# Optimization experiments

Measured on AMD Instinct MI355X. Metric: run time of the kernel, lower is better.

## Reference

```python
import jax, jax.numpy as jnp
import numpy as np

VOCAB, X_SIZE, H_SIZE, N_CLASSES = 50000, 300, 150, 5
DEPTH = 18                      # complete binary tree, N = 2^(DEPTH+1)-1 nodes
N_NODES = 2 ** (DEPTH + 1) - 1  # 524287
SCALE = 0.05                    # param init scale for numerical sanity


def setup_inputs() -> dict:
    key = jax.random.key(0)
    ks = jax.random.split(key, 8)
    return {
        "x_id": jax.random.randint(ks[0], (N_NODES,), 0, VOCAB, dtype=jnp.int32),
        "emb": jax.random.normal(ks[1], (VOCAB, X_SIZE), jnp.float32) * SCALE,
        "W_iou": jax.random.normal(ks[2], (X_SIZE, 3 * H_SIZE), jnp.float32) * SCALE,
        "U_iou": jax.random.normal(ks[3], (H_SIZE, 3 * H_SIZE), jnp.float32) * SCALE,
        "b_iou": jnp.zeros((3 * H_SIZE,), jnp.float32),
        "W_f": jax.random.normal(ks[4], (X_SIZE, H_SIZE), jnp.float32) * SCALE,
        "U_f": jax.random.normal(ks[5], (H_SIZE, H_SIZE), jnp.float32) * SCALE,
        "b_f": jnp.zeros((H_SIZE,), jnp.float32),
        "W_out": jax.random.normal(ks[6], (H_SIZE, N_CLASSES), jnp.float32) * SCALE,
        "b_out": jnp.zeros((N_CLASSES,), jnp.float32),
    }


def reference(x_id, emb, W_iou, U_iou, b_iou, W_f, U_f, b_f, W_out, b_out):
    # Child-Sum TreeLSTM propagated leaves->root over a complete binary tree
    # stored in heap layout: children of node i are 2i+1, 2i+2.
    N = x_id.shape[0]
    H = U_iou.shape[0]
    depth = int(np.log2(N + 1)) - 1

    x = emb[x_id]  # input_module: embedding lookup  [N, X]
    h = jnp.zeros((N, H), x.dtype)
    c = jnp.zeros((N, H), x.dtype)

    # level-batched topological propagation (19 static levels)
    for lvl in range(depth, -1, -1):
        s, e = 2 ** lvl - 1, 2 ** (lvl + 1) - 1  # node range of this level
        xl = x[s:e]                              # [n_l, X]
        if lvl == depth:  # leaves: zero child state
            h_sum = jnp.zeros((e - s, H), x.dtype)
            fc_sum = jnp.zeros((e - s, H), x.dtype)
        else:
            # children of consecutive nodes are contiguous: [2s+1, 2e+1)
            hc = h[2 * s + 1:2 * e + 1].reshape(e - s, 2, H)
            cc = c[2 * s + 1:2 * e + 1].reshape(e - s, 2, H)
            h_sum = hc.sum(axis=1)               # reduce: sum child h
            # per-child forget gate
            f = jax.nn.sigmoid((xl @ W_f)[:, None, :] + hc @ U_f + b_f)
            fc_sum = (f * cc).sum(axis=1)
        iou = xl @ W_iou + h_sum @ U_iou + b_iou  # [n_l, 3H]
        i, o, u = jnp.split(iou, 3, axis=-1)
        c_new = jax.nn.sigmoid(i) * jnp.tanh(u) + fc_sum
        h_new = jax.nn.sigmoid(o) * jnp.tanh(c_new)
        h = h.at[s:e].set(h_new)
        c = c.at[s:e].set(c_new)

    return h @ W_out + b_out  # output_module: Linear(H, C)  [N, C]
```

## Files before the change

### kernel.cpp

```cpp
#include <hip/hip_runtime.h>
#include <cstdint>

typedef _Float16 f16_t;
typedef __attribute__((ext_vector_type(8))) _Float16 f16x8;
typedef __attribute__((ext_vector_type(4))) _Float16 f16x4;
typedef __attribute__((ext_vector_type(4))) float f32x4;

#define HP      160
#define NCOL    640
#define KXP     320
#define LEAF_S  262143
#define NVOCAB  50000
#define AST     168
#define BST     36
#define CST     162

__device__ __forceinline__ float frcp(float x) { return __builtin_amdgcn_rcpf(x); }
__device__ __forceinline__ float sigf(float x) { return frcp(1.0f + __expf(-x)); }
__device__ __forceinline__ float tanhf_(float x) {
  return 1.0f - 2.0f * frcp(1.0f + __expf(2.0f * x));
}
__device__ __forceinline__ f16x8 zero8() {
  f16x8 z;
#pragma unroll
  for (int i = 0; i < 8; ++i) z[i] = (_Float16)0.0f;
  return z;
}
__device__ __forceinline__ f32x4 zero4() {
  f32x4 z;
#pragma unroll
  for (int i = 0; i < 4; ++i) z[i] = 0.0f;
  return z;
}

__device__ __forceinline__ void stage_B(const f16_t* __restrict__ UreT, f16_t* B_sh,
                                        int tid, int j0, int kk) {
#pragma unroll
  for (int i = 0; i < 2; ++i) {
    int ch = tid + 256 * i;
    int cidx = ch >> 2, kc = (ch & 3) * 8;
    int g = cidx >> 5, jj = cidx & 31;
    int col = g * HP + j0 + jj;
    f16x8 v = *(const f16x8*)&UreT[col * HP + kk + kc];
    f16x4 lo = {v[0], v[1], v[2], v[3]};
    f16x4 hi = {v[4], v[5], v[6], v[7]};
    *(f16x4*)&B_sh[cidx * BST + kc] = lo;
    *(f16x4*)&B_sh[cidx * BST + kc + 4] = hi;
  }
}
__device__ __forceinline__ f16x8 read_B(const f16_t* B_sh, int tile16, int q) {
  f16x4 lo = *(const f16x4*)&B_sh[tile16 * BST + q * 8];
  f16x4 hi = *(const f16x4*)&B_sh[tile16 * BST + q * 8 + 4];
  f16x8 v = {lo[0], lo[1], lo[2], lo[3], hi[0], hi[1], hi[2], hi[3]};
  return v;
}

__global__ void prep_params(const float* __restrict__ W_iou, const float* __restrict__ U_iou,
                            const float* __restrict__ b_iou, const float* __restrict__ W_f,
                            const float* __restrict__ U_f, const float* __restrict__ b_f,
                            f16_t* __restrict__ WreT, f16_t* __restrict__ UreT,
                            float* __restrict__ bre) {
  int idx = blockIdx.x * 256 + threadIdx.x;
  if (idx < NCOL * KXP) {
    int col = idx / KXP, k = idx % KXP;
    int j = col >> 2, g = col & 3;
    float v = 0.0f;
    if (k < 300 && j < 150) v = (g < 3) ? W_iou[k * 450 + g * 150 + j] : W_f[k * 150 + j];
    WreT[idx] = (f16_t)v;
  } else if (idx < NCOL * KXP + NCOL * HP) {
    int i2 = idx - NCOL * KXP;
    int col = i2 / HP, k = i2 % HP;
    int g = col / 160, j = col % 160;
    float v = 0.0f;
    if (k < 150 && j < 150) v = (g < 3) ? U_iou[k * 450 + g * 150 + j] : U_f[k * 150 + j];
    UreT[i2] = (f16_t)v;
  } else if (idx < NCOL * KXP + NCOL * HP + NCOL) {
    int col = idx - (NCOL * KXP + NCOL * HP);
    int j = col >> 2, g = col & 3;
    bre[col] = (j < 150) ? ((g < 3) ? b_iou[g * 150 + j] : b_f[j]) : 0.0f;
  }
}

__global__ __launch_bounds__(256) void gemm_p(const float* __restrict__ emb,
                                              const f16_t* __restrict__ WreT,
                                              const float* __restrict__ bre,
                                              f16_t* __restrict__ P) {
  __shared__ __align__(16) f16_t A_sh[64 * 328];
  __shared__ __align__(16) f16_t B_sh[128 * 40];
  const int tid = threadIdx.x;
  const int wid = tid >> 6, lane = tid & 63, l15 = lane & 15, q = lane >> 4;
  const int row0 = blockIdx.x * 64;

#pragma unroll
  for (int i = 0; i < 10; ++i) {
    int ch = tid + 256 * i;
    int r = ch / 40, kc = (ch % 40) * 8;
    int grow = row0 + r;
    f16x8 hv;
    if (grow < NVOCAB && kc + 8 <= 300) {
      float4 a = *(const float4*)&emb[grow * 300 + kc];
      float4 b = *(const float4*)&emb[grow * 300 + kc + 4];
      hv[0] = (_Float16)a.x; hv[1] = (_Float16)a.y; hv[2] = (_Float16)a.z; hv[3] = (_Float16)a.w;
      hv[4] = (_Float16)b.x; hv[5] = (_Float16)b.y; hv[6] = (_Float16)b.z; hv[7] = (_Float16)b.w;
    } else {
#pragma unroll
      for (int e = 0; e < 8; ++e) {
        int k = kc + e;
        float v = (grow < NVOCAB && k < 300) ? emb[grow * 300 + k] : 0.0f;
        hv[e] = (_Float16)v;
      }
    }
    *(f16x8*)&A_sh[r * 328 + kc] = hv;
  }
  __syncthreads();

  for (int bn = 0; bn < 5; ++bn) {
    const int col0 = bn * 128;
    f32x4 acc[8];
#pragma unroll
    for (int t = 0; t < 8; ++t) acc[t] = zero4();
    for (int kk = 0; kk < KXP; kk += 32) {
#pragma unroll
      for (int i = 0; i < 2; ++i) {
        int ch = tid + 256 * i;
        int cidx = ch >> 2, kc = (ch & 3) * 8;
        *(f16x8*)&B_sh[cidx * 40 + kc] =
            *(const f16x8*)&WreT[(col0 + cidx) * KXP + kk + kc];
      }
      __syncthreads();
      f16x8 af = *(const f16x8*)&A_sh[(16 * wid + l15) * 328 + kk + q * 8];
#pragma unroll
      for (int t = 0; t < 8; ++t) {
        f16x8 bfr = *(const f16x8*)&B_sh[(t * 16 + l15) * 40 + q * 8];
        acc[t] = __builtin_amdgcn_mfma_f32_16x16x32_f16(af, bfr, acc[t], 0, 0, 0);
      }
      __syncthreads();
    }
#pragma unroll
    for (int t = 0; t < 8; ++t) {
      int col = col0 + t * 16 + l15;
      float bias = bre[col];
#pragma unroll
      for (int r2 = 0; r2 < 4; ++r2) {
        int row = row0 + 16 * wid + q * 4 + r2;
        if (row < NVOCAB) P[(long)row * NCOL + col] = (f16_t)(acc[t][r2] + bias);
      }
    }
  }
}

__global__ void leafhc_kernel(const f16_t* __restrict__ P, f16_t* __restrict__ Hleaf,
                              f16_t* __restrict__ Cleaf) {
  int idx = blockIdx.x * 256 + threadIdx.x;
  if (idx >= NVOCAB * 80) return;
  int v = idx / 80, t = idx % 80;
  f16x8 pk = *(const f16x8*)&P[(long)v * NCOL + t * 8];
#pragma unroll
  for (int e = 0; e < 2; ++e) {
    float iv = (float)pk[e * 4 + 0], ov = (float)pk[e * 4 + 1], uv = (float)pk[e * 4 + 2];
    float cl = sigf(iv) * tanhf_(uv);
    float hl = sigf(ov) * tanhf_(cl);
    Hleaf[(long)v * HP + t * 2 + e] = (f16_t)hl;
    Cleaf[(long)v * HP + t * 2 + e] = (f16_t)cl;
  }
}

__global__ __launch_bounds__(256, 4) void fused17_kernel(
    const int* __restrict__ x_id, const f16_t* __restrict__ P,
    const f16_t* __restrict__ UreT, const f16_t* __restrict__ Hleaf,
    const f16_t* __restrict__ Cleaf, f16_t* __restrict__ Hout,
    f16_t* __restrict__ Cout, const float* __restrict__ W_out,
    const float* __restrict__ b_out, float* __restrict__ out) {
  __shared__ __align__(16) f16_t B_sh[128 * BST];
  __shared__ __align__(16) f16_t A2_sh[32 * AST];
  __shared__ f16_t C_sh[32 * CST];
  __shared__ __align__(16) f16_t Wo16[160 * 8];
  const int tid = threadIdx.x;
  const int wid = tid >> 6, lane = tid & 63, l15 = lane & 15, q = lane >> 4;
  const int p0 = blockIdx.x * 32;
  const int s1 = (1 << 17) - 1;
  const long childbase = (long)LEAF_S + 2 * p0;

  for (int idx = tid; idx < 1280; idx += 256) {
    int j = idx >> 3, m = idx & 7;
    Wo16[idx] = (j < 150 && m < 5) ? (f16_t)W_out[j * 5 + m] : (f16_t)0.0f;
  }

  const int row = 16 * wid + l15;
  const int xvrow = x_id[childbase + row];
  const f16_t* hrow = Hleaf + (long)xvrow * HP;
  f16x8 areg[5];
#pragma unroll
  for (int kx = 0; kx < 5; ++kx) areg[kx] = *(const f16x8*)&hrow[kx * 32 + q * 8];

  int xvp[2], xvl[2], xvr[2];
#pragma unroll
  for (int rr = 0; rr < 2; ++rr) {
    int pl = 8 * wid + 2 * q + rr;
    xvp[rr] = x_id[(long)s1 + p0 + pl];
    xvl[rr] = x_id[childbase + 2 * pl];
    xvr[rr] = x_id[childbase + 2 * pl + 1];
  }
  __syncthreads();

  {
    float o[5] = {0, 0, 0, 0, 0};
#pragma unroll
    for (int kx = 0; kx < 5; ++kx)
#pragma unroll
      for (int e = 0; e < 8; ++e) {
        int j = kx * 32 + q * 8 + e;
        float hv = (float)areg[kx][e];
        f16x8 w8 = *(const f16x8*)&Wo16[j * 8];
#pragma unroll
        for (int m = 0; m < 5; ++m) o[m] += hv * (float)w8[m];
      }
#pragma unroll
    for (int m = 0; m < 5; ++m) {
      float v = o[m];
      v += __shfl_xor(v, 16);
      v += __shfl_xor(v, 32);
      o[m] = v;
    }
    if (q == 0) {
      long base = (childbase + row) * 5;
#pragma unroll
      for (int m = 0; m < 5; ++m) out[base + m] = o[m] + b_out[m];
    }
  }

  float oacc1[2][5] = {};
  for (int jt = 0; jt < 5; ++jt) {
    const int j0 = jt * 32;
    f32x4 acc[4][2];
#pragma unroll
    for (int g = 0; g < 4; ++g)
#pragma unroll
      for (int jh = 0; jh < 2; ++jh) acc[g][jh] = zero4();

    for (int kx = 0; kx < 5; ++kx) {
      stage_B(UreT, B_sh, tid, j0, kx * 32);
      __syncthreads();
#pragma unroll
      for (int g = 0; g < 4; ++g)
#pragma unroll
        for (int jh = 0; jh < 2; ++jh) {
          f16x8 bfr = read_B(B_sh, g * 32 + jh * 16 + l15, q);
          acc[g][jh] = __builtin_amdgcn_mfma_f32_16x16x32_f16(areg[kx], bfr, acc[g][jh], 0, 0, 0);
        }
      __syncthreads();
    }

#pragma unroll
    for (int rr = 0; rr < 2; ++rr) {
      const int r = rr * 2;
      const int pl = 8 * wid + 2 * q + rr;
      const f16_t* Prp = P + (long)xvp[rr] * NCOL;
      const f16_t* Crl = Cleaf + (long)xvl[rr] * HP;
      const f16_t* Crr = Cleaf + (long)xvr[rr] * HP;
#pragma unroll
      for (int jh = 0; jh < 2; ++jh) {
        const int j = j0 + jh * 16 + l15;
        f16x4 pp = *(const f16x4*)&Prp[j * 4];
        float ipre = (float)pp[0] + acc[0][jh][r] + acc[0][jh][r + 1];
        float opre = (float)pp[1] + acc[1][jh][r] + acc[1][jh][r + 1];
        float upre = (float)pp[2] + acc[2][jh][r] + acc[2][jh][r + 1];
        float pf   = (float)pp[3];
        float fl = sigf(pf + acc[3][jh][r]);
        float fr = sigf(pf + acc[3][jh][r + 1]);
        float cn = sigf(ipre) * tanhf_(upre) + fl * (float)Crl[j] + fr * (float)Crr[j];
        float hn = sigf(opre) * tanhf_(cn);
        A2_sh[pl * AST + j] = (f16_t)hn;
        C_sh[pl * CST + j] = (f16_t)cn;
        f16x8 w8 = *(const f16x8*)&Wo16[j * 8];
#pragma unroll
        for (int m = 0; m < 5; ++m) oacc1[rr][m] += hn * (float)w8[m];
      }
    }
  }
  __syncthreads();

#pragma unroll
  for (int rr = 0; rr < 2; ++rr) {
    const int pl = 8 * wid + 2 * q + rr;
#pragma unroll
    for (int m = 0; m < 5; ++m) {
      float v = oacc1[rr][m];
      v += __shfl_xor(v, 1);
      v += __shfl_xor(v, 2);
      v += __shfl_xor(v, 4);
      v += __shfl_xor(v, 8);
      if (l15 == 0) out[((long)s1 + p0 + pl) * 5 + m] = v + b_out[m];
    }
  }

  const int s2 = (s1 - 1) >> 1;
  const int p02 = p0 >> 1;
  const bool act2 = (wid < 2);
  f16x8 a2reg[5];
  if (act2) {
#pragma unroll
    for (int kx = 0; kx < 5; ++kx)
      a2reg[kx] = *(const f16x8*)&A2_sh[(16 * wid + l15) * AST + kx * 32 + q * 8];
  }
  int xvp2[2];
#pragma unroll
  for (int rr = 0; rr < 2; ++rr) {
    int pl = 8 * wid + 2 * q + rr;
    xvp2[rr] = x_id[(long)s2 + p02 + (act2 ? pl : 0)];
  }

  float oacc2[2][5] = {};
  for (int jt = 0; jt < 5; ++jt) {
    const int j0 = jt * 32;
    f32x4 acc[4][2];
#pragma unroll
    for (int g = 0; g < 4; ++g)
#pragma unroll
      for (int jh = 0; jh < 2; ++jh) acc[g][jh] = zero4();

    for (int kx = 0; kx < 5; ++kx) {
      stage_B(UreT, B_sh, tid, j0, kx * 32);
      __syncthreads();
      if (act2) {
#pragma unroll
        for (int g = 0; g < 4; ++g)
#pragma unroll
          for (int jh = 0; jh < 2; ++jh) {
            f16x8 bfr = read_B(B_sh, g * 32 + jh * 16 + l15, q);
            acc[g][jh] = __builtin_amdgcn_mfma_f32_16x16x32_f16(a2reg[kx], bfr, acc[g][jh], 0, 0, 0);
          }
      }
      __syncthreads();
    }

    if (act2) {
#pragma unroll
      for (int rr = 0; rr < 2; ++rr) {
        const int r = rr * 2;
        const int lr0 = 16 * wid + q * 4 + r;
        const int pl = lr0 >> 1;
        const f16_t* Prp = P + (long)xvp2[rr] * NCOL;
#pragma unroll
        for (int jh = 0; jh < 2; ++jh) {
          const int j = j0 + jh * 16 + l15;
          f16x4 pp = *(const f16x4*)&Prp[j * 4];
          float ipre = (float)pp[0] + acc[0][jh][r] + acc[0][jh][r + 1];
          float opre = (float)pp[1] + acc[1][jh][r] + acc[1][jh][r + 1];
          float upre = (float)pp[2] + acc[2][jh][r] + acc[2][jh][r + 1];
          float pf   = (float)pp[3];
          float fl = sigf(pf + acc[3][jh][r]);
          float fr = sigf(pf + acc[3][jh][r + 1]);
          float cn = sigf(ipre) * tanhf_(upre) +
                     fl * (float)C_sh[lr0 * CST + j] + fr * (float)C_sh[(lr0 + 1) * CST + j];
          float hn = sigf(opre) * tanhf_(cn);
          Hout[(long)(p02 + pl) * HP + j] = (f16_t)hn;
          Cout[(long)(p02 + pl) * HP + j] = (f16_t)cn;
          f16x8 w8 = *(const f16x8*)&Wo16[j * 8];
#pragma unroll
          for (int m = 0; m < 5; ++m) oacc2[rr][m] += hn * (float)w8[m];
        }
      }
    }
  }

  if (act2) {
#pragma unroll
    for (int rr = 0; rr < 2; ++rr) {
      const int pl = 8 * wid + 2 * q + rr;
#pragma unroll
      for (int m = 0; m < 5; ++m) {
        float v = oacc2[rr][m];
        v += __shfl_xor(v, 1);
        v += __shfl_xor(v, 2);
        v += __shfl_xor(v, 4);
        v += __shfl_xor(v, 8);
        if (l15 == 0) out[((long)s2 + p02 + pl) * 5 + m] = v + b_out[m];
      }
    }
  }
}

__global__ __launch_bounds__(256, 4) void level_k(
    const int* __restrict__ x_id, const f16_t* __restrict__ P,
    const f16_t* __restrict__ UreT, const f16_t* __restrict__ Hc,
    const f16_t* __restrict__ Cc, f16_t* __restrict__ Hp,
    f16_t* __restrict__ Cp, const float* __restrict__ W_out,
    const float* __restrict__ b_out, float* __restrict__ out, int s, int M) {
  __shared__ __align__(16) f16_t B_sh[128 * BST];
  __shared__ __align__(16) f16_t Wo16[160 * 8];
  const int tid = threadIdx.x;
  const int wid = tid >> 6, lane = tid & 63, l15 = lane & 15, q = lane >> 4;
  const int p0 = blockIdx.x * 32;

  for (int idx = tid; idx < 1280; idx += 256) {
    int j = idx >> 3, m = idx & 7;
    Wo16[idx] = (j < 150 && m < 5) ? (f16_t)W_out[j * 5 + m] : (f16_t)0.0f;
  }

  const int row = 16 * wid + l15;
  const f16_t* hrow = Hc + (long)(2 * p0 + row) * HP;
  f16x8 areg[5];
#pragma unroll
  for (int kx = 0; kx < 5; ++kx) areg[kx] = *(const f16x8*)&hrow[kx * 32 + q * 8];

  int xvp[2];
#pragma unroll
  for (int rr = 0; rr < 2; ++rr) {
    int pl = 8 * wid + 2 * q + rr;
    xvp[rr] = x_id[(long)s + p0 + pl];
  }
  __syncthreads();

  float oacc[2][5] = {};
  for (int jt = 0; jt < 5; ++jt) {
    const int j0 = jt * 32;
    f32x4 acc[4][2];
#pragma unroll
    for (int g = 0; g < 4; ++g)
#pragma unroll
      for (int jh = 0; jh < 2; ++jh) acc[g][jh] = zero4();

    for (int kx = 0; kx < 5; ++kx) {
      stage_B(UreT, B_sh, tid, j0, kx * 32);
      __syncthreads();
#pragma unroll
      for (int g = 0; g < 4; ++g)
#pragma unroll
        for (int jh = 0; jh < 2; ++jh) {
          f16x8 bfr = read_B(B_sh, g * 32 + jh * 16 + l15, q);
          acc[g][jh] = __builtin_amdgcn_mfma_f32_16x16x32_f16(areg[kx], bfr, acc[g][jh], 0, 0, 0);
        }
      __syncthreads();
    }

#pragma unroll
    for (int rr = 0; rr < 2; ++rr) {
      const int r = rr * 2;
      const int lr0 = 16 * wid + q * 4 + r;
      const int pl = lr0 >> 1;
      const f16_t* Prp = P + (long)xvp[rr] * NCOL;
#pragma unroll
      for (int jh = 0; jh < 2; ++jh) {
        const int j = j0 + jh * 16 + l15;
        f16x4 pp = *(const f16x4*)&Prp[j * 4];
        float ipre = (float)pp[0] + acc[0][jh][r] + acc[0][jh][r + 1];
        float opre = (float)pp[1] + acc[1][jh][r] + acc[1][jh][r + 1];
        float upre = (float)pp[2] + acc[2][jh][r] + acc[2][jh][r + 1];
        float pf   = (float)pp[3];
        float fl = sigf(pf + acc[3][jh][r]);
        float fr = sigf(pf + acc[3][jh][r + 1]);
        float clv = (float)Cc[(long)(2 * p0 + lr0) * HP + j];
        float crv = (float)Cc[(long)(2 * p0 + lr0 + 1) * HP + j];
        float cn = sigf(ipre) * tanhf_(upre) + fl * clv + fr * crv;
        float hn = sigf(opre) * tanhf_(cn);
        Hp[(long)(p0 + pl) * HP + j] = (f16_t)hn;
        Cp[(long)(p0 + pl) * HP + j] = (f16_t)cn;
        f16x8 w8 = *(const f16x8*)&Wo16[j * 8];
#pragma unroll
        for (int m = 0; m < 5; ++m) oacc[rr][m] += hn * (float)w8[m];
      }
    }
  }

#pragma unroll
  for (int rr = 0; rr < 2; ++rr) {
    const int pl = 8 * wid + 2 * q + rr;
#pragma unroll
    for (int m = 0; m < 5; ++m) {
      float v = oacc[rr][m];
      v += __shfl_xor(v, 1);
      v += __shfl_xor(v, 2);
      v += __shfl_xor(v, 4);
      v += __shfl_xor(v, 8);
      if (l15 == 0) out[((long)s + p0 + pl) * 5 + m] = v + b_out[m];
    }
  }
}

__global__ __launch_bounds__(256, 4) void tail_kernel(
    const int* __restrict__ x_id, const f16_t* __restrict__ P,
    const f16_t* __restrict__ UreT, f16_t* __restrict__ HX, f16_t* __restrict__ HY,
    f16_t* __restrict__ CX, f16_t* __restrict__ CY, const float* __restrict__ W_out,
    const float* __restrict__ b_out, float* __restrict__ out) {
  __shared__ __align__(16) f16_t B_sh[128 * BST];
  __shared__ __align__(16) f16_t Wo16[160 * 8];
  const int tid = threadIdx.x;
  const int wid = tid >> 6, lane = tid & 63, l15 = lane & 15, q = lane >> 4;

  for (int idx = tid; idx < 1280; idx += 256) {
    int j = idx >> 3, m = idx & 7;
    Wo16[idx] = (j < 150 && m < 5) ? (f16_t)W_out[j * 5 + m] : (f16_t)0.0f;
  }

  for (int lvl = 5; lvl >= 0; --lvl) {
    const int s = (1 << lvl) - 1, M = 1 << lvl;
    const f16_t* hc = (lvl & 1) ? HX : HY;
    const f16_t* cc = (lvl & 1) ? CX : CY;
    f16_t* hp = (lvl & 1) ? HY : HX;
    f16_t* cp = (lvl & 1) ? CY : CX;
    int rowsValid = 2 * M;
    if (rowsValid > 64) rowsValid = 64;

    __threadfence();
    __syncthreads();

    const int row = 16 * wid + l15;
    f16x8 areg[5];
#pragma unroll
    for (int kx = 0; kx < 5; ++kx)
      areg[kx] = (row < rowsValid) ? *(const f16x8*)&hc[(long)row * HP + kx * 32 + q * 8]
                                   : zero8();

    int xvp[2]; bool valid[2];
#pragma unroll
    for (int rr = 0; rr < 2; ++rr) {
      int pl = 8 * wid + 2 * q + rr;
      valid[rr] = pl < M;
      xvp[rr] = x_id[(long)s + (valid[rr] ? pl : 0)];
    }

    float oacc[2][5] = {};
    for (int jt = 0; jt < 5; ++jt) {
      const int j0 = jt * 32;
      f32x4 acc[4][2];
#pragma unroll
      for (int g = 0; g < 4; ++g)
#pragma unroll
        for (int jh = 0; jh < 2; ++jh) acc[g][jh] = zero4();

      for (int kx = 0; kx < 5; ++kx) {
        stage_B(UreT, B_sh, tid, j0, kx * 32);
        __syncthreads();
#pragma unroll
        for (int g = 0; g < 4; ++g)
#pragma unroll
          for (int jh = 0; jh < 2; ++jh) {
            f16x8 bfr = read_B(B_sh, g * 32 + jh * 16 + l15, q);
            acc[g][jh] = __builtin_amdgcn_mfma_f32_16x16x32_f16(areg[kx], bfr, acc[g][jh], 0, 0, 0);
          }
        __syncthreads();
      }

#pragma unroll
      for (int rr = 0; rr < 2; ++rr) {
        const int r = rr * 2;
        const int lr0 = 16 * wid + q * 4 + r;
        const int pl = lr0 >> 1;
        const f16_t* Prp = P + (long)xvp[rr] * NCOL;
#pragma unroll
        for (int jh = 0; jh < 2; ++jh) {
          const int j = j0 + jh * 16 + l15;
          f16x4 pp = *(const f16x4*)&Prp[j * 4];
          float ipre = (float)pp[0] + acc[0][jh][r] + acc[0][jh][r + 1];
          float opre = (float)pp[1] + acc[1][jh][r] + acc[1][jh][r + 1];
          float upre = (float)pp[2] + acc[2][jh][r] + acc[2][jh][r + 1];
          float pf   = (float)pp[3];
          float fl = sigf(pf + acc[3][jh][r]);
          float fr = sigf(pf + acc[3][jh][r + 1]);
          float clv = valid[rr] ? (float)cc[(long)lr0 * HP + j] : 0.0f;
          float crv = valid[rr] ? (float)cc[(long)(lr0 + 1) * HP + j] : 0.0f;
          float cn = sigf(ipre) * tanhf_(upre) + fl * clv + fr * crv;
          float hn = sigf(opre) * tanhf_(cn);
          if (valid[rr]) {
            hp[(long)pl * HP + j] = (f16_t)hn;
            cp[(long)pl * HP + j] = (f16_t)cn;
          }
          f16x8 w8 = *(const f16x8*)&Wo16[j * 8];
#pragma unroll
          for (int m = 0; m < 5; ++m) oacc[rr][m] += hn * (float)w8[m];
        }
      }
    }

#pragma unroll
    for (int rr = 0; rr < 2; ++rr) {
      const int pl = 8 * wid + 2 * q + rr;
#pragma unroll
      for (int m = 0; m < 5; ++m) {
        float v = oacc[rr][m];
        v += __shfl_xor(v, 1);
        v += __shfl_xor(v, 2);
        v += __shfl_xor(v, 4);
        v += __shfl_xor(v, 8);
        if (l15 == 0 && valid[rr]) out[((long)s + pl) * 5 + m] = v + b_out[m];
      }
    }
  }
}

extern "C" void kernel_launch(void* const* d_in, const int* in_sizes, int n_in,
                              void* d_out, int out_size, void* d_ws, size_t ws_size,
                              hipStream_t stream) {
  const int* x_id   = (const int*)d_in[0];
  const float* emb  = (const float*)d_in[1];
  const float* W_iou = (const float*)d_in[2];
  const float* U_iou = (const float*)d_in[3];
  const float* b_iou = (const float*)d_in[4];
  const float* W_f   = (const float*)d_in[5];
  const float* U_f   = (const float*)d_in[6];
  const float* b_f   = (const float*)d_in[7];
  const float* W_out = (const float*)d_in[8];
  const float* b_out = (const float*)d_in[9];
  float* out = (float*)d_out;
  char* ws = (char*)d_ws;

  f16_t* WreT  = (f16_t*)(ws + 0);
  f16_t* UreT  = (f16_t*)(ws + 409600);
  float* bre   = (float*)(ws + 614400);
  f16_t* P     = (f16_t*)(ws + 616960);
  f16_t* Hleaf = (f16_t*)(ws + 64616960);
  f16_t* Cleaf = (f16_t*)(ws + 80616960);
  f16_t* HX    = (f16_t*)(ws + 96616960);
  f16_t* HY    = (f16_t*)(ws + 117588480);
  f16_t* CX    = (f16_t*)(ws + 138560000);
  f16_t* CY    = (f16_t*)(ws + 159531520);

  prep_params<<<1203, 256, 0, stream>>>(W_iou, U_iou, b_iou, W_f, U_f, b_f, WreT, UreT, bre);
  gemm_p<<<782, 256, 0, stream>>>(emb, WreT, bre, P);
  leafhc_kernel<<<15625, 256, 0, stream>>>(P, Hleaf, Cleaf);

  fused17_kernel<<<4096, 256, 0, stream>>>(x_id, P, UreT, Hleaf, Cleaf, HX, CX,
                                           W_out, b_out, out);

  for (int L = 15; L >= 6; --L) {
    int s = (1 << L) - 1, M = 1 << L;
    const f16_t* hc = (L & 1) ? HX : HY;
    const f16_t* cc = (L & 1) ? CX : CY;
    f16_t* hp = (L & 1) ? HY : HX;
    f16_t* cp = (L & 1) ? CY : CX;
    level_k<<<M / 32, 256, 0, stream>>>(x_id, P, UreT, hc, cc, hp, cp,
                                        W_out, b_out, out, s, M);
  }

  tail_kernel<<<1, 256, 0, stream>>>(x_id, P, UreT, HX, HY, CX, CY, W_out, b_out, out);

  (void)in_sizes; (void)n_in; (void)out_size; (void)ws_size;
}
```

Baseline: 885.1 us.

## Stage larger K-slabs of weights in LDS to cut barrier count

Result: slower. 980.4 us (+10.8%).

```diff
diff --git a/kernel.cpp b/kernel.cpp
--- a/kernel.cpp
+++ b/kernel.cpp
@@ -8,12 +8,12 @@
 
 #define HP      160
 #define NCOL    640
-#define KXP     320
 #define LEAF_S  262143
 #define NVOCAB  50000
-#define AST     168
-#define BST     36
+#define A2ST    168
 #define CST     162
+#define BSTL    168
+#define BSTF    104
 
 __device__ __forceinline__ float frcp(float x) { return __builtin_amdgcn_rcpf(x); }
 __device__ __forceinline__ float sigf(float x) { return frcp(1.0f + __expf(-x)); }
@@ -31,28 +31,6 @@
 #pragma unroll
   for (int i = 0; i < 4; ++i) z[i] = 0.0f;
   return z;
-}
-
-__device__ __forceinline__ void stage_B(const f16_t* __restrict__ UreT, f16_t* B_sh,
-                                        int tid, int j0, int kk) {
-#pragma unroll
-  for (int i = 0; i < 2; ++i) {
-    int ch = tid + 256 * i;
-    int cidx = ch >> 2, kc = (ch & 3) * 8;
-    int g = cidx >> 5, jj = cidx & 31;
-    int col = g * HP + j0 + jj;
-    f16x8 v = *(const f16x8*)&UreT[col * HP + kk + kc];
-    f16x4 lo = {v[0], v[1], v[2], v[3]};
-    f16x4 hi = {v[4], v[5], v[6], v[7]};
-    *(f16x4*)&B_sh[cidx * BST + kc] = lo;
-    *(f16x4*)&B_sh[cidx * BST + kc + 4] = hi;
-  }
-}
-__device__ __forceinline__ f16x8 read_B(const f16_t* B_sh, int tile16, int q) {
-  f16x4 lo = *(const f16x4*)&B_sh[tile16 * BST + q * 8];
-  f16x4 hi = *(const f16x4*)&B_sh[tile16 * BST + q * 8 + 4];
-  f16x8 v = {lo[0], lo[1], lo[2], lo[3], hi[0], hi[1], hi[2], hi[3]};
-  return v;
 }
 
 __global__ void prep_params(const float* __restrict__ W_iou, const float* __restrict__ U_iou,
@@ -61,78 +39,79 @@
                             f16_t* __restrict__ WreT, f16_t* __restrict__ UreT,
                             float* __restrict__ bre) {
   int idx = blockIdx.x * 256 + threadIdx.x;
-  if (idx < NCOL * KXP) {
-    int col = idx / KXP, k = idx % KXP;
+  if (idx < NCOL * 320) {
+    int col = idx / 320, k = idx % 320;
     int j = col >> 2, g = col & 3;
     float v = 0.0f;
     if (k < 300 && j < 150) v = (g < 3) ? W_iou[k * 450 + g * 150 + j] : W_f[k * 150 + j];
     WreT[idx] = (f16_t)v;
-  } else if (idx < NCOL * KXP + NCOL * HP) {
-    int i2 = idx - NCOL * KXP;
+  } else if (idx < NCOL * 320 + NCOL * HP) {
+    int i2 = idx - NCOL * 320;
     int col = i2 / HP, k = i2 % HP;
     int g = col / 160, j = col % 160;
     float v = 0.0f;
     if (k < 150 && j < 150) v = (g < 3) ? U_iou[k * 450 + g * 150 + j] : U_f[k * 150 + j];
     UreT[i2] = (f16_t)v;
-  } else if (idx < NCOL * KXP + NCOL * HP + NCOL) {
-    int col = idx - (NCOL * KXP + NCOL * HP);
+  } else if (idx < NCOL * 320 + NCOL * HP + NCOL) {
+    int col = idx - (NCOL * 320 + NCOL * HP);
     int j = col >> 2, g = col & 3;
     bre[col] = (j < 150) ? ((g < 3) ? b_iou[g * 150 + j] : b_f[j]) : 0.0f;
   }
 }
 
-__global__ __launch_bounds__(256) void gemm_p(const float* __restrict__ emb,
-                                              const f16_t* __restrict__ WreT,
-                                              const float* __restrict__ bre,
-                                              f16_t* __restrict__ P) {
-  __shared__ __align__(16) f16_t A_sh[64 * 328];
-  __shared__ __align__(16) f16_t B_sh[128 * 40];
+__global__ __launch_bounds__(256, 3) void gemm_p(const float* __restrict__ emb,
+                                                 const f16_t* __restrict__ WreT,
+                                                 const float* __restrict__ bre,
+                                                 f16_t* __restrict__ P) {
+  __shared__ __align__(16) f16_t B_sh[128 * BSTL];
   const int tid = threadIdx.x;
   const int wid = tid >> 6, lane = tid & 63, l15 = lane & 15, q = lane >> 4;
   const int row0 = blockIdx.x * 64;
-
-#pragma unroll
-  for (int i = 0; i < 10; ++i) {
-    int ch = tid + 256 * i;
-    int r = ch / 40, kc = (ch % 40) * 8;
-    int grow = row0 + r;
-    f16x8 hv;
-    if (grow < NVOCAB && kc + 8 <= 300) {
-      float4 a = *(const float4*)&emb[grow * 300 + kc];
-      float4 b = *(const float4*)&emb[grow * 300 + kc + 4];
-      hv[0] = (_Float16)a.x; hv[1] = (_Float16)a.y; hv[2] = (_Float16)a.z; hv[3] = (_Float16)a.w;
-      hv[4] = (_Float16)b.x; hv[5] = (_Float16)b.y; hv[6] = (_Float16)b.z; hv[7] = (_Float16)b.w;
-    } else {
-#pragma unroll
-      for (int e = 0; e < 8; ++e) {
-        int k = kc + e;
-        float v = (grow < NVOCAB && k < 300) ? emb[grow * 300 + k] : 0.0f;
-        hv[e] = (_Float16)v;
-      }
-    }
-    *(f16x8*)&A_sh[r * 328 + kc] = hv;
-  }
-  __syncthreads();
+  const int row = row0 + 16 * wid + l15;
+
+  f16x8 areg[10];
+#pragma unroll
+  for (int kx = 0; kx < 10; ++kx) {
+    int k0 = kx * 32 + q * 8;
+    f16x8 hv = zero8();
+    if (row < NVOCAB) {
+      if (k0 + 8 <= 300) {
+        float4 a = *(const float4*)&emb[row * 300 + k0];
+        float4 b = *(const float4*)&emb[row * 300 + k0 + 4];
+        hv[0] = (_Float16)a.x; hv[1] = (_Float16)a.y; hv[2] = (_Float16)a.z; hv[3] = (_Float16)a.w;
+        hv[4] = (_Float16)b.x; hv[5] = (_Float16)b.y; hv[6] = (_Float16)b.z; hv[7] = (_Float16)b.w;
+      } else {
+#pragma unroll
+        for (int e = 0; e < 8; ++e)
+          hv[e] = (k0 + e < 300) ? (_Float16)emb[row * 300 + k0 + e] : (_Float16)0.0f;
+      }
+    }
+    areg[kx] = hv;
+  }
 
   for (int bn = 0; bn < 5; ++bn) {
     const int col0 = bn * 128;
     f32x4 acc[8];
 #pragma unroll
     for (int t = 0; t < 8; ++t) acc[t] = zero4();
-    for (int kk = 0; kk < KXP; kk += 32) {
-#pragma unroll
-      for (int i = 0; i < 2; ++i) {
-        int ch = tid + 256 * i;
-        int cidx = ch >> 2, kc = (ch & 3) * 8;
-        *(f16x8*)&B_sh[cidx * 40 + kc] =
-            *(const f16x8*)&WreT[(col0 + cidx) * KXP + kk + kc];
+
+    for (int ks = 0; ks < 2; ++ks) {
+#pragma unroll
+      for (int i = 0; i < 10; ++i) {
+        int c2 = tid + 256 * i;
+        int col = c2 / 20, kc8 = (c2 % 20) * 8;
+        *(f16x8*)&B_sh[col * BSTL + kc8] =
+            *(const f16x8*)&WreT[(col0 + col) * 320 + ks * 160 + kc8];
       }
       __syncthreads();
-      f16x8 af = *(const f16x8*)&A_sh[(16 * wid + l15) * 328 + kk + q * 8];
-#pragma unroll
-      for (int t = 0; t < 8; ++t) {
-        f16x8 bfr = *(const f16x8*)&B_sh[(t * 16 + l15) * 40 + q * 8];
-        acc[t] = __builtin_amdgcn_mfma_f32_16x16x32_f16(af, bfr, acc[t], 0, 0, 0);
+#pragma unroll
+      for (int kx = 0; kx < 5; ++kx) {
+        f16x8 af = areg[ks * 5 + kx];
+#pragma unroll
+        for (int t = 0; t < 8; ++t) {
+          f16x8 bfr = *(const f16x8*)&B_sh[(t * 16 + l15) * BSTL + kx * 32 + q * 8];
+          acc[t] = __builtin_amdgcn_mfma_f32_16x16x32_f16(af, bfr, acc[t], 0, 0, 0);
+        }
       }
       __syncthreads();
     }
@@ -142,8 +121,8 @@
       float bias = bre[col];
 #pragma unroll
       for (int r2 = 0; r2 < 4; ++r2) {
-        int row = row0 + 16 * wid + q * 4 + r2;
-        if (row < NVOCAB) P[(long)row * NCOL + col] = (f16_t)(acc[t][r2] + bias);
+        int orow = row0 + 16 * wid + q * 4 + r2;
+        if (orow < NVOCAB) P[(long)orow * NCOL + col] = (f16_t)(acc[t][r2] + bias);
       }
     }
   }
@@ -165,16 +144,16 @@
   }
 }
 
-__global__ __launch_bounds__(256, 4) void fused17_kernel(
+__global__ __launch_bounds__(256, 3) void fused17_kernel(
     const int* __restrict__ x_id, const f16_t* __restrict__ P,
     const f16_t* __restrict__ UreT, const f16_t* __restrict__ Hleaf,
     const f16_t* __restrict__ Cleaf, f16_t* __restrict__ Hout,
     f16_t* __restrict__ Cout, const float* __restrict__ W_out,
     const float* __restrict__ b_out, float* __restrict__ out) {
-  __shared__ __align__(16) f16_t B_sh[128 * BST];
-  __shared__ __align__(16) f16_t A2_sh[32 * AST];
+  __shared__ __align__(16) f16_t B_sh[128 * BSTF];
+  __shared__ __align__(16) f16_t A2_sh[32 * A2ST];
   __shared__ f16_t C_sh[32 * CST];
-  __shared__ __align__(16) f16_t Wo16[160 * 8];
+  __shared__ __align__(16) f16_t Wo16[1280];
   const int tid = threadIdx.x;
   const int wid = tid >> 6, lane = tid & 63, l15 = lane & 15, q = lane >> 4;
   const int p0 = blockIdx.x * 32;
@@ -238,18 +217,44 @@
 #pragma unroll
       for (int jh = 0; jh < 2; ++jh) acc[g][jh] = zero4();
 
-    for (int kx = 0; kx < 5; ++kx) {
-      stage_B(UreT, B_sh, tid, j0, kx * 32);
-      __syncthreads();
+#pragma unroll
+    for (int i = 0; i < 6; ++i) {
+      int c2 = tid + 256 * i;
+      int col = c2 / 12, kc8 = (c2 % 12) * 8;
+      int g = col >> 5, jj = col & 31;
+      *(f16x8*)&B_sh[col * BSTF + kc8] =
+          *(const f16x8*)&UreT[(g * HP + j0 + jj) * HP + kc8];
+    }
+    __syncthreads();
+#pragma unroll
+    for (int kx = 0; kx < 3; ++kx)
 #pragma unroll
       for (int g = 0; g < 4; ++g)
 #pragma unroll
         for (int jh = 0; jh < 2; ++jh) {
-          f16x8 bfr = read_B(B_sh, g * 32 + jh * 16 + l15, q);
+          f16x8 bfr = *(const f16x8*)&B_sh[(g * 32 + jh * 16 + l15) * BSTF + kx * 32 + q * 8];
           acc[g][jh] = __builtin_amdgcn_mfma_f32_16x16x32_f16(areg[kx], bfr, acc[g][jh], 0, 0, 0);
         }
-      __syncthreads();
-    }
+    __syncthreads();
+#pragma unroll
+    for (int i = 0; i < 4; ++i) {
+      int c2 = tid + 256 * i;
+      int col = c2 >> 3, kc8 = (c2 & 7) * 8;
+      int g = col >> 5, jj = col & 31;
+      *(f16x8*)&B_sh[col * BSTF + kc8] =
+          *(const f16x8*)&UreT[(g * HP + j0 + jj) * HP + 96 + kc8];
+    }
+    __syncthreads();
+#pragma unroll
+    for (int kx = 0; kx < 2; ++kx)
+#pragma unroll
+      for (int g = 0; g < 4; ++g)
+#pragma unroll
+        for (int jh = 0; jh < 2; ++jh) {
+          f16x8 bfr = *(const f16x8*)&B_sh[(g * 32 + jh * 16 + l15) * BSTF + kx * 32 + q * 8];
+          acc[g][jh] = __builtin_amdgcn_mfma_f32_16x16x32_f16(areg[3 + kx], bfr, acc[g][jh], 0, 0, 0);
+        }
+    __syncthreads();
 
 #pragma unroll
     for (int rr = 0; rr < 2; ++rr) {
@@ -270,7 +275,7 @@
         float fr = sigf(pf + acc[3][jh][r + 1]);
         float cn = sigf(ipre) * tanhf_(upre) + fl * (float)Crl[j] + fr * (float)Crr[j];
         float hn = sigf(opre) * tanhf_(cn);
-        A2_sh[pl * AST + j] = (f16_t)hn;
+        A2_sh[pl * A2ST + j] = (f16_t)hn;
         C_sh[pl * CST + j] = (f16_t)cn;
         f16x8 w8 = *(const f16x8*)&Wo16[j * 8];
 #pragma unroll
@@ -301,7 +306,7 @@
   if (act2) {
 #pragma unroll
     for (int kx = 0; kx < 5; ++kx)
-      a2reg[kx] = *(const f16x8*)&A2_sh[(16 * wid + l15) * AST + kx * 32 + q * 8];
+      a2reg[kx] = *(const f16x8*)&A2_sh[(16 * wid + l15) * A2ST + kx * 32 + q * 8];
   }
   int xvp2[2];
 #pragma unroll
@@ -319,20 +324,48 @@
 #pragma unroll
       for (int jh = 0; jh < 2; ++jh) acc[g][jh] = zero4();
 
-    for (int kx = 0; kx < 5; ++kx) {
-      stage_B(UreT, B_sh, tid, j0, kx * 32);
-      __syncthreads();
-      if (act2) {
+#pragma unroll
+    for (int i = 0; i < 6; ++i) {
+      int c2 = tid + 256 * i;
+      int col = c2 / 12, kc8 = (c2 % 12) * 8;
+      int g = col >> 5, jj = col & 31;
+      *(f16x8*)&B_sh[col * BSTF + kc8] =
+          *(const f16x8*)&UreT[(g * HP + j0 + jj) * HP + kc8];
+    }
+    __syncthreads();
+    if (act2) {
+#pragma unroll
+      for (int kx = 0; kx < 3; ++kx)
 #pragma unroll
         for (int g = 0; g < 4; ++g)
 #pragma unroll
           for (int jh = 0; jh < 2; ++jh) {
-            f16x8 bfr = read_B(B_sh, g * 32 + jh * 16 + l15, q);
+            f16x8 bfr = *(const f16x8*)&B_sh[(g * 32 + jh * 16 + l15) * BSTF + kx * 32 + q * 8];
             acc[g][jh] = __builtin_amdgcn_mfma_f32_16x16x32_f16(a2reg[kx], bfr, acc[g][jh], 0, 0, 0);
           }
-      }
-      __syncthreads();
-    }
+    }
+    __syncthreads();
+#pragma unroll
+    for (int i = 0; i < 4; ++i) {
+      int c2 = tid + 256 * i;
+      int col = c2 >> 3, kc8 = (c2 & 7) * 8;
+      int g = col >> 5, jj = col & 31;
+      *(f16x8*)&B_sh[col * BSTF + kc8] =
+          *(const f16x8*)&UreT[(g * HP + j0 + jj) * HP + 96 + kc8];
+    }
+    __syncthreads();
+    if (act2) {
+#pragma unroll
+      for (int kx = 0; kx < 2; ++kx)
+#pragma unroll
+        for (int g = 0; g < 4; ++g)
+#pragma unroll
+          for (int jh = 0; jh < 2; ++jh) {
+            f16x8 bfr = *(const f16x8*)&B_sh[(g * 32 + jh * 16 + l15) * BSTF + kx * 32 + q * 8];
+            acc[g][jh] = __builtin_amdgcn_mfma_f32_16x16x32_f16(a2reg[3 + kx], bfr, acc[g][jh], 0, 0, 0);
+          }
+    }
+    __syncthreads();
 
     if (act2) {
 #pragma unroll
@@ -381,14 +414,14 @@
   }
 }
 
-__global__ __launch_bounds__(256, 4) void level_k(
+__global__ __launch_bounds__(256, 3) void level_k(
     const int* __restrict__ x_id, const f16_t* __restrict__ P,
     const f16_t* __restrict__ UreT, const f16_t* __restrict__ Hc,
     const f16_t* __restrict__ Cc, f16_t* __restrict__ Hp,
     f16_t* __restrict__ Cp, const float* __restrict__ W_out,
     const float* __restrict__ b_out, float* __restrict__ out, int s, int M) {
-  __shared__ __align__(16) f16_t B_sh[128 * BST];
-  __shared__ __align__(16) f16_t Wo16[160 * 8];
+  __shared__ __align__(16) f16_t B_sh[128 * BSTL];
+  __shared__ __align__(16) f16_t Wo16[1280];
   const int tid = threadIdx.x;
   const int wid = tid >> 6, lane = tid & 63, l15 = lane & 15, q = lane >> 4;
   const int p0 = blockIdx.x * 32;
@@ -410,7 +443,6 @@
     int pl = 8 * wid + 2 * q + rr;
     xvp[rr] = x_id[(long)s + p0 + pl];
   }
-  __syncthreads();
 
   float oacc[2][5] = {};
   for (int jt = 0; jt < 5; ++jt) {
@@ -421,18 +453,25 @@
 #pragma unroll
       for (int jh = 0; jh < 2; ++jh) acc[g][jh] = zero4();
 
-    for (int kx = 0; kx < 5; ++kx) {
-      stage_B(UreT, B_sh, tid, j0, kx * 32);
-      __syncthreads();
+#pragma unroll
+    for (int i = 0; i < 10; ++i) {
+      int c2 = tid + 256 * i;
+      int col = c2 / 20, kc8 = (c2 % 20) * 8;
+      int g = col >> 5, jj = col & 31;
+      *(f16x8*)&B_sh[col * BSTL + kc8] =
+          *(const f16x8*)&UreT[(g * HP + j0 + jj) * HP + kc8];
+    }
+    __syncthreads();
+#pragma unroll
+    for (int kx = 0; kx < 5; ++kx)
 #pragma unroll
       for (int g = 0; g < 4; ++g)
 #pragma unroll
         for (int jh = 0; jh < 2; ++jh) {
-          f16x8 bfr = read_B(B_sh, g * 32 + jh * 16 + l15, q);
+          f16x8 bfr = *(const f16x8*)&B_sh[(g * 32 + jh * 16 + l15) * BSTL + kx * 32 + q * 8];
           acc[g][jh] = __builtin_amdgcn_mfma_f32_16x16x32_f16(areg[kx], bfr, acc[g][jh], 0, 0, 0);
         }
-      __syncthreads();
-    }
+    __syncthreads();
 
 #pragma unroll
     for (int rr = 0; rr < 2; ++rr) {
@@ -478,13 +517,13 @@
   }
 }
 
-__global__ __launch_bounds__(256, 4) void tail_kernel(
+__global__ __launch_bounds__(256, 3) void tail_kernel(
     const int* __restrict__ x_id, const f16_t* __restrict__ P,
     const f16_t* __restrict__ UreT, f16_t* __restrict__ HX, f16_t* __restrict__ HY,
     f16_t* __restrict__ CX, f16_t* __restrict__ CY, const float* __restrict__ W_out,
     const float* __restrict__ b_out, float* __restrict__ out) {
-  __shared__ __align__(16) f16_t B_sh[128 * BST];
-  __shared__ __align__(16) f16_t Wo16[160 * 8];
+  __shared__ __align__(16) f16_t B_sh[128 * BSTL];
+  __shared__ __align__(16) f16_t Wo16[1280];
   const int tid = threadIdx.x;
   const int wid = tid >> 6, lane = tid & 63, l15 = lane & 15, q = lane >> 4;
 
@@ -529,18 +568,25 @@
 #pragma unroll
         for (int jh = 0; jh < 2; ++jh) acc[g][jh] = zero4();
 
-      for (int kx = 0; kx < 5; ++kx) {
-        stage_B(UreT, B_sh, tid, j0, kx * 32);
-        __syncthreads();
+#pragma unroll
+      for (int i = 0; i < 10; ++i) {
+        int c2 = tid + 256 * i;
+        int col = c2 / 20, kc8 = (c2 % 20) * 8;
+        int g = col >> 5, jj = col & 31;
+        *(f16x8*)&B_sh[col * BSTL + kc8] =
+            *(const f16x8*)&UreT[(g * HP + j0 + jj) * HP + kc8];
+      }
+      __syncthreads();
+#pragma unroll
+      for (int kx = 0; kx < 5; ++kx)
 #pragma unroll
         for (int g = 0; g < 4; ++g)
 #pragma unroll
           for (int jh = 0; jh < 2; ++jh) {
-            f16x8 bfr = read_B(B_sh, g * 32 + jh * 16 + l15, q);
+            f16x8 bfr = *(const f16x8*)&B_sh[(g * 32 + jh * 16 + l15) * BSTL + kx * 32 + q * 8];
             acc[g][jh] = __builtin_amdgcn_mfma_f32_16x16x32_f16(areg[kx], bfr, acc[g][jh], 0, 0, 0);
           }
-        __syncthreads();
-      }
+      __syncthreads();
 
 #pragma unroll
       for (int rr = 0; rr < 2; ++rr) {
```
